# Optimization experiments

Hardware: AMD Instinct MI355X
Metric: run time of the kernel (lower is better)

The kernel has to match this reference:

```python
import jax, jax.numpy as jnp
import numpy as np


def bin_op_s(a, b, w):
    """Differentiable weighted sum over the 16 real-valued binary logic gates.
    a, b: [B, O] soft-boolean inputs; w: [O, 16] gate mixture weights.
    Gate order matches difflogic's bin_op_s.
    """
    ab = a * b
    a_plus_b = a + b
    one = jnp.asarray(1.0, a.dtype)
    # w[:, i] broadcasts [O] against [B, O]
    return (
        # w[:, 0] * 0 (FALSE) contributes nothing
        w[:, 1] * ab                              # a AND b
        + w[:, 2] * (a - ab)                      # a AND NOT b
        + w[:, 3] * a                             # a
        + w[:, 4] * (b - ab)                      # NOT a AND b
        + w[:, 5] * b                             # b
        + w[:, 6] * (a_plus_b - 2.0 * ab)         # a XOR b
        + w[:, 7] * (a_plus_b - ab)               # a OR b
        + w[:, 8] * (one - (a_plus_b - ab))       # NOR
        + w[:, 9] * (one - (a_plus_b - 2.0 * ab)) # XNOR
        + w[:, 10] * (one - b)                    # NOT b
        + w[:, 11] * (one - b + ab)               # b -> a
        + w[:, 12] * (one - a)                    # NOT a
        + w[:, 13] * (one - a + ab)               # a -> b
        + w[:, 14] * (one - ab)                   # NAND
        + w[:, 15] * one                          # TRUE
    )


def setup_inputs() -> dict:
    key = jax.random.key(0)
    k_x, k_w, k_a, k_b = jax.random.split(key, 4)
    B, IN_DIM, OUT_DIM = 2048, 8192, 16384
    x = jax.random.uniform(k_x, (B, IN_DIM), dtype=jnp.float32)
    weights = jax.random.normal(k_w, (OUT_DIM, 16), dtype=jnp.float32)
    idx_a = jax.random.randint(k_a, (OUT_DIM,), 0, IN_DIM, dtype=jnp.int64 if jax.config.jax_enable_x64 else jnp.int32)
    idx_b = jax.random.randint(k_b, (OUT_DIM,), 0, IN_DIM, dtype=jnp.int64 if jax.config.jax_enable_x64 else jnp.int32)
    return {"x": x, "weights": weights, "idx_a": idx_a, "idx_b": idx_b}


def reference(x, weights, idx_a, idx_b):
    # training-mode forward_python: gather the two connected inputs per neuron,
    # softmax the 16 gate logits, and take the soft gate mixture.
    a = x[:, idx_a]  # [B, out_dim]
    b = x[:, idx_b]  # [B, out_dim]
    w = jax.nn.softmax(weights, axis=-1)  # [out_dim, 16]
    return bin_op_s(a, b, w)
```

## Files before the change

### kernel.cpp

```cpp
#include <hip/hip_runtime.h>


#define THREADS 256
#define IN_DIM_MAX 8192

__global__ __launch_bounds__(THREADS) void coeffs_k(
    const float* __restrict__ w,
    float4* __restrict__ cf,
    int OUT_DIM)
{
    const int j = blockIdx.x * THREADS + threadIdx.x;
    if (j >= OUT_DIM) return;

    float wv[16];
    const float4* wp = reinterpret_cast<const float4*>(w + (size_t)j * 16);
    #pragma unroll
    for (int q = 0; q < 4; ++q) {
        float4 v = wp[q];
        wv[q * 4 + 0] = v.x;
        wv[q * 4 + 1] = v.y;
        wv[q * 4 + 2] = v.z;
        wv[q * 4 + 3] = v.w;
    }

    float m = -1e30f;
    #pragma unroll
    for (int g = 0; g < 16; ++g) m = fmaxf(m, wv[g]);

    float e[16];
    float s = 0.f;
    #pragma unroll
    for (int g = 0; g < 16; ++g) {
        e[g] = __expf(wv[g] - m);
        s += e[g];
    }
    const float inv = 1.f / s;

    const float C0  = e[8] + e[9] + e[10] + e[11] + e[12] + e[13] + e[14] + e[15];
    const float Ca  = e[2] + e[3] + e[6] + e[7] - e[8] - e[9] - e[12] - e[13];
    const float Cb  = e[4] + e[5] + e[6] + e[7] - e[8] - e[9] - e[10] - e[11];
    const float Cab = e[1] - e[2] - e[4] - 2.f * e[6] - e[7]
                    + e[8] + 2.f * e[9] + e[11] + e[13] - e[14];

    cf[j] = make_float4(C0 * inv, Ca * inv, Cb * inv, Cab * inv);
}

__global__ __launch_bounds__(THREADS) void row_k(
    const float* __restrict__ x,
    const float4* __restrict__ cf,
    const int4* __restrict__ ia4,
    const int4* __restrict__ ib4,
    float4* __restrict__ out4,
    int IN_DIM, int OUT_DIM)
{
    __shared__ float sx[IN_DIM_MAX];

    const int row = blockIdx.x;
    const int tid = threadIdx.x;

    {
        const float4* xr4 = reinterpret_cast<const float4*>(x + (size_t)row * IN_DIM);
        float4* s4 = reinterpret_cast<float4*>(sx);
        const int n4 = IN_DIM / 4;
        #pragma unroll 2
        for (int t = tid; t < n4; t += THREADS) s4[t] = xr4[t];
    }
    __syncthreads();

    float4* __restrict__ orow = out4 + (size_t)row * (OUT_DIM / 4);
    const int nchunk = OUT_DIM / (THREADS * 4);

    #pragma unroll 2
    for (int c = 0; c < nchunk; ++c) {
        const int j4 = c * THREADS + tid;
        const int j  = j4 * 4;

        const int4 va = ia4[j4];
        const int4 vb = ib4[j4];
        const float4 f0 = cf[j + 0];
        const float4 f1 = cf[j + 1];
        const float4 f2 = cf[j + 2];
        const float4 f3 = cf[j + 3];

        float4 r;
        {
            const float a = sx[va.x], b = sx[vb.x];
            r.x = fmaf(a * b, f0.w, fmaf(b, f0.z, fmaf(a, f0.y, f0.x)));
        }
        {
            const float a = sx[va.y], b = sx[vb.y];
            r.y = fmaf(a * b, f1.w, fmaf(b, f1.z, fmaf(a, f1.y, f1.x)));
        }
        {
            const float a = sx[va.z], b = sx[vb.z];
            r.z = fmaf(a * b, f2.w, fmaf(b, f2.z, fmaf(a, f2.y, f2.x)));
        }
        {
            const float a = sx[va.w], b = sx[vb.w];
            r.w = fmaf(a * b, f3.w, fmaf(b, f3.z, fmaf(a, f3.y, f3.x)));
        }
        orow[j4] = r;
    }
}

extern "C" void kernel_launch(void* const* d_in, const int* in_sizes, int n_in,
                              void* d_out, int out_size, void* d_ws, size_t ws_size,
                              hipStream_t stream) {
    const float* x     = (const float*)d_in[0];
    const float* w     = (const float*)d_in[1];
    const int*   idx_a = (const int*)d_in[2];
    const int*   idx_b = (const int*)d_in[3];
    float*       out   = (float*)d_out;

    const int OUT_DIM = in_sizes[2];
    const int B       = out_size / OUT_DIM;
    const int IN_DIM  = in_sizes[0] / B;

    float4* cf = (float4*)d_ws;

    coeffs_k<<<(OUT_DIM + THREADS - 1) / THREADS, THREADS, 0, stream>>>(
        w, cf, OUT_DIM);

    row_k<<<B, THREADS, 0, stream>>>(
        x, cf,
        reinterpret_cast<const int4*>(idx_a),
        reinterpret_cast<const int4*>(idx_b),
        reinterpret_cast<float4*>(out),
        IN_DIM, OUT_DIM);
}
```

Baseline: 223.6 us.

## Process two rows per block, split coefficients into SoA, prefetch next chunk

```diff
diff --git a/kernel.cpp b/kernel.cpp
--- a/kernel.cpp
+++ b/kernel.cpp
@@ -2,11 +2,13 @@
 
 
 #define THREADS 256
-#define IN_DIM_MAX 8192
+#define ROWS 2
+#define IN_DIM_C 8192
 
 __global__ __launch_bounds__(THREADS) void coeffs_k(
     const float* __restrict__ w,
-    float4* __restrict__ cf,
+    float* __restrict__ c0o, float* __restrict__ cao,
+    float* __restrict__ cbo, float* __restrict__ cabo,
     int OUT_DIM)
 {
     const int j = blockIdx.x * THREADS + threadIdx.x;
@@ -17,23 +19,17 @@
     #pragma unroll
     for (int q = 0; q < 4; ++q) {
         float4 v = wp[q];
-        wv[q * 4 + 0] = v.x;
-        wv[q * 4 + 1] = v.y;
-        wv[q * 4 + 2] = v.z;
-        wv[q * 4 + 3] = v.w;
+        wv[q * 4 + 0] = v.x; wv[q * 4 + 1] = v.y;
+        wv[q * 4 + 2] = v.z; wv[q * 4 + 3] = v.w;
     }
 
     float m = -1e30f;
     #pragma unroll
     for (int g = 0; g < 16; ++g) m = fmaxf(m, wv[g]);
 
-    float e[16];
-    float s = 0.f;
+    float e[16]; float s = 0.f;
     #pragma unroll
-    for (int g = 0; g < 16; ++g) {
-        e[g] = __expf(wv[g] - m);
-        s += e[g];
-    }
+    for (int g = 0; g < 16; ++g) { e[g] = __expf(wv[g] - m); s += e[g]; }
     const float inv = 1.f / s;
 
     const float C0  = e[8] + e[9] + e[10] + e[11] + e[12] + e[13] + e[14] + e[15];
@@ -42,64 +38,79 @@
     const float Cab = e[1] - e[2] - e[4] - 2.f * e[6] - e[7]
                     + e[8] + 2.f * e[9] + e[11] + e[13] - e[14];
 
-    cf[j] = make_float4(C0 * inv, Ca * inv, Cb * inv, Cab * inv);
+    c0o[j]  = C0  * inv;
+    cao[j]  = Ca  * inv;
+    cbo[j]  = Cb  * inv;
+    cabo[j] = Cab * inv;
 }
 
 __global__ __launch_bounds__(THREADS) void row_k(
     const float* __restrict__ x,
-    const float4* __restrict__ cf,
+    const float4* __restrict__ c04, const float4* __restrict__ ca4,
+    const float4* __restrict__ cb4, const float4* __restrict__ cab4,
     const int4* __restrict__ ia4,
     const int4* __restrict__ ib4,
     float4* __restrict__ out4,
     int IN_DIM, int OUT_DIM)
 {
-    __shared__ float sx[IN_DIM_MAX];
+    __shared__ float sx[ROWS * IN_DIM_C];
 
-    const int row = blockIdx.x;
-    const int tid = threadIdx.x;
+    const int row0 = blockIdx.x * ROWS;
+    const int tid  = threadIdx.x;
+    const int nchunk = OUT_DIM / (THREADS * 4);
+
+    int4   va = ia4[tid];
+    int4   vb = ib4[tid];
+    float4 f0 = c04[tid], fa = ca4[tid], fb = cb4[tid], fc = cab4[tid];
 
     {
-        const float4* xr4 = reinterpret_cast<const float4*>(x + (size_t)row * IN_DIM);
+        const float4* xr4 = reinterpret_cast<const float4*>(x + (size_t)row0 * IN_DIM);
         float4* s4 = reinterpret_cast<float4*>(sx);
-        const int n4 = IN_DIM / 4;
-        #pragma unroll 2
+        const int n4 = ROWS * IN_DIM / 4;
+        #pragma unroll
         for (int t = tid; t < n4; t += THREADS) s4[t] = xr4[t];
     }
     __syncthreads();
 
-    float4* __restrict__ orow = out4 + (size_t)row * (OUT_DIM / 4);
-    const int nchunk = OUT_DIM / (THREADS * 4);
+    const int o4 = OUT_DIM / 4;
+    float4* __restrict__ orow0 = out4 + (size_t)row0 * o4;
+    float4* __restrict__ orow1 = orow0 + o4;
 
-    #pragma unroll 2
+    #pragma unroll 1
     for (int c = 0; c < nchunk; ++c) {
+        const int4   cva = va, cvb = vb;
+        const float4 g0 = f0, ga = fa, gb = fb, gc = fc;
         const int j4 = c * THREADS + tid;
-        const int j  = j4 * 4;
 
-        const int4 va = ia4[j4];
-        const int4 vb = ib4[j4];
-        const float4 f0 = cf[j + 0];
-        const float4 f1 = cf[j + 1];
-        const float4 f2 = cf[j + 2];
-        const float4 f3 = cf[j + 3];
+        if (c + 1 < nchunk) {
+            const int nj4 = j4 + THREADS;
+            va = ia4[nj4]; vb = ib4[nj4];
+            f0 = c04[nj4]; fa = ca4[nj4]; fb = cb4[nj4]; fc = cab4[nj4];
+        }
 
-        float4 r;
+        float4 r0, r1;
         {
-            const float a = sx[va.x], b = sx[vb.x];
-            r.x = fmaf(a * b, f0.w, fmaf(b, f0.z, fmaf(a, f0.y, f0.x)));
+            const float a0 = sx[cva.x], b0 = sx[cvb.x];
+            const float a1 = sx[cva.y], b1 = sx[cvb.y];
+            const float a2 = sx[cva.z], b2 = sx[cvb.z];
+            const float a3 = sx[cva.w], b3 = sx[cvb.w];
+            r0.x = fmaf(a0 * b0, gc.x, fmaf(b0, gb.x, fmaf(a0, ga.x, g0.x)));
+            r0.y = fmaf(a1 * b1, gc.y, fmaf(b1, gb.y, fmaf(a1, ga.y, g0.y)));
+            r0.z = fmaf(a2 * b2, gc.z, fmaf(b2, gb.z, fmaf(a2, ga.z, g0.z)));
+            r0.w = fmaf(a3 * b3, gc.w, fmaf(b3, gb.w, fmaf(a3, ga.w, g0.w)));
         }
         {
-            const float a = sx[va.y], b = sx[vb.y];
-            r.y = fmaf(a * b, f1.w, fmaf(b, f1.z, fmaf(a, f1.y, f1.x)));
+            const float a0 = sx[IN_DIM_C + cva.x], b0 = sx[IN_DIM_C + cvb.x];
+            const float a1 = sx[IN_DIM_C + cva.y], b1 = sx[IN_DIM_C + cvb.y];
+            const float a2 = sx[IN_DIM_C + cva.z], b2 = sx[IN_DIM_C + cvb.z];
+            const float a3 = sx[IN_DIM_C + cva.w], b3 = sx[IN_DIM_C + cvb.w];
+            r1.x = fmaf(a0 * b0, gc.x, fmaf(b0, gb.x, fmaf(a0, ga.x, g0.x)));
+            r1.y = fmaf(a1 * b1, gc.y, fmaf(b1, gb.y, fmaf(a1, ga.y, g0.y)));
+            r1.z = fmaf(a2 * b2, gc.z, fmaf(b2, gb.z, fmaf(a2, ga.z, g0.z)));
+            r1.w = fmaf(a3 * b3, gc.w, fmaf(b3, gb.w, fmaf(a3, ga.w, g0.w)));
         }
-        {
-            const float a = sx[va.z], b = sx[vb.z];
-            r.z = fmaf(a * b, f2.w, fmaf(b, f2.z, fmaf(a, f2.y, f2.x)));
-        }
-        {
-            const float a = sx[va.w], b = sx[vb.w];
-            r.w = fmaf(a * b, f3.w, fmaf(b, f3.z, fmaf(a, f3.y, f3.x)));
-        }
-        orow[j4] = r;
+        orow0[j4] = r0;
+        orow1[j4] = r1;
     }
 }
 
@@ -116,13 +127,20 @@
     const int B       = out_size / OUT_DIM;
     const int IN_DIM  = in_sizes[0] / B;
 
-    float4* cf = (float4*)d_ws;
+    float* c0  = (float*)d_ws;
+    float* ca  = c0 + OUT_DIM;
+    float* cb  = ca + OUT_DIM;
+    float* cab = cb + OUT_DIM;
 
     coeffs_k<<<(OUT_DIM + THREADS - 1) / THREADS, THREADS, 0, stream>>>(
-        w, cf, OUT_DIM);
+        w, c0, ca, cb, cab, OUT_DIM);
 
-    row_k<<<B, THREADS, 0, stream>>>(
-        x, cf,
+    row_k<<<B / ROWS, THREADS, 0, stream>>>(
+        x,
+        reinterpret_cast<const float4*>(c0),
+        reinterpret_cast<const float4*>(ca),
+        reinterpret_cast<const float4*>(cb),
+        reinterpret_cast<const float4*>(cab),
         reinterpret_cast<const int4*>(idx_a),
         reinterpret_cast<const int4*>(idx_b),
         reinterpret_cast<float4*>(out),
```

Measured after the change: 201.5 us. 1.11x faster.
